# Kernel tuning notes

Hardware: AMD Instinct MI355X
Metric: run time of the kernel (lower is better)

Reference implementation:

```python
import jax, jax.numpy as jnp
import numpy as np

B, N, C, H = 16, 577, 768, 12
KEEP_RATE = 0.7


def setup_inputs() -> dict:
    key = jax.random.key(0)
    k1, k2, k3 = jax.random.split(key, 3)
    x = jax.random.normal(k1, (B, N, C), dtype=jnp.float32)
    W_qkv = jax.random.normal(k2, (C, 3 * C), dtype=jnp.float32) * 0.02
    W_proj = jax.random.normal(k3, (C, C), dtype=jnp.float32) * 0.02
    b_proj = jnp.zeros((C,), dtype=jnp.float32)
    return {"x": x, "W_qkv": W_qkv, "W_proj": W_proj, "b_proj": b_proj}


def reference(x, W_qkv, W_proj, b_proj):
    b, n, c = x.shape
    h = H
    dh = c // h
    scale = dh ** (-0.5)

    # qkv projection -> q,k,v each [B,H,N,dh]
    qkv = (x @ W_qkv).reshape(b, n, 3, h, dh)
    qkv = jnp.transpose(qkv, (2, 0, 3, 1, 4))
    q, k, v = qkv[0], qkv[1], qkv[2]

    # full attention scores [B,H,N,N] (materialized, as in the source)
    attn = jnp.einsum('bhnd,bhmd->bhnm', q, k) * scale

    # --- top_pool from row-0 (CLS) scores, attn_method == 'SUM_ABS_1' ---
    # attn[:, :, 0, :] -> [B,H,N]; sum |.| over heads -> [B,N] (== mean over C=1 channel)
    attn_weight = jnp.sum(jnp.abs(attn[:, :, 0, :]), axis=1)  # [B,N]
    # exclude_first=True: drop CLS, topk over remaining N-1, alpha1=1, alpha2=0 (C==1 -> std=0)
    w = attn_weight[:, 1:]                       # [B, N-1]
    keep_num = max(int((n - 1) * KEEP_RATE), 1)  # static
    _, idx = jax.lax.top_k(w, keep_num)          # [B, keep_num]
    idx = jnp.sort(idx, axis=1)
    idx = jnp.concatenate(
        [jnp.zeros((b, 1), dtype=idx.dtype), idx + 1], axis=1)  # prepend CLS index 0
    # expand to [B, keep_num+1, dim] as in torch (pool dim kwarg == self.dim)
    keep_index = jnp.broadcast_to(idx[:, :, None], (b, keep_num + 1, c))

    # standard attention output
    a = jax.nn.softmax(attn, axis=-1)
    out = jnp.einsum('bhnm,bhmd->bhnd', a, v)    # [B,H,N,dh]
    out = jnp.transpose(out, (0, 2, 1, 3)).reshape(b, n, c)
    out = out @ W_proj + b_proj
    return out, keep_index
```

## Files before the change

### kernel.cpp

```cpp
#include <hip/hip_runtime.h>
#include <hip/hip_bf16.h>
#include <stdint.h>

#define B_    16
#define N_    577
#define C_    768
#define H_    12
#define M_    (B_*N_)
#define QKVN  (3*C_)
#define NKEEP 403
#define KROWS (NKEEP+1)
#define VTLD  640
#define PTLD  72

typedef short s16x8 __attribute__((ext_vector_type(8)));
typedef float f32x4 __attribute__((ext_vector_type(4)));

__device__ __forceinline__ unsigned short f2bf(float x){
  unsigned int u = __float_as_uint(x);
  u += 0x7FFF + ((u >> 16) & 1);
  return (unsigned short)(u >> 16);
}

__device__ __forceinline__ void gld_lds16(const void* g, void* l){
  __builtin_amdgcn_global_load_lds(
      (const __attribute__((address_space(1))) unsigned int*)g,
      (__attribute__((address_space(3))) unsigned int*)l, 16, 0, 0);
}

template<int NT, int M9, int MTILES>
__device__ __forceinline__ void tile_map(int L, int& mt, int& nt){
  constexpr int NB = MTILES*NT;
  int x = L & 7, j = L >> 3;
  if(j < M9*NT){
    nt = j/M9; mt = x*M9 + (j - nt*M9);
  } else {
    int offt = 0;
    #pragma unroll
    for(int y=0;y<8;y++) if(y<x) offt += ((NB-1-y)>>3) + 1 - M9*NT;
    int ft = offt + (j - M9*NT);
    mt = 8*M9 + ft/NT;
    nt = ft - (ft/NT)*NT;
  }
}

__global__ __launch_bounds__(256) void k_prep(const float* __restrict__ x,
                       const float* __restrict__ Wqkv, const float* __restrict__ Wproj,
                       unsigned short* __restrict__ xb, unsigned short* __restrict__ wqkvT,
                       unsigned short* __restrict__ wprojT, float* __restrict__ qcls){
  __shared__ float tile[64][65];
  __shared__ float part[4][64];
  const int bid = blockIdx.x, t = threadIdx.x;
  if(bid < 6924){
    int i = bid*256 + t;
    float4 v = ((const float4*)x)[i];
    ushort4 o; o.x=f2bf(v.x); o.y=f2bf(v.y); o.z=f2bf(v.z); o.w=f2bf(v.w);
    ((ushort4*)xb)[i] = o;
  } else if(bid < 7500){
    const float* in; unsigned short* out; int R, CC, bx, by;
    if(bid < 7356){ int r = bid - 6924; bx = r % 36; by = r / 36; in = Wqkv;  out = wqkvT;  R = 768; CC = 2304; }
    else          { int r = bid - 7356; bx = r % 12; by = r / 12; in = Wproj; out = wprojT; R = 768; CC = 768;  }
    int r0 = by*64, c0 = bx*64;
    int tx = t & 63, ty = t >> 6;
    #pragma unroll
    for(int i=0;i<16;i++){
      int r = ty + i*4;
      tile[r][tx] = in[(size_t)(r0+r)*CC + c0 + tx];
    }
    __syncthreads();
    #pragma unroll
    for(int i=0;i<16;i++){
      int c = ty + i*4;
      out[(size_t)(c0+c)*R + r0 + tx] = f2bf(tile[tx][c]);
    }
  } else {
    int r = bid - 7500;
    const int b = r / 12, j0 = (r % 12)*64;
    float* xs = &tile[0][0];
    const float* xr = x + (size_t)b*577*768;
    xs[t] = xr[t]; xs[t+256] = xr[t+256]; xs[t+512] = xr[t+512];
    __syncthreads();
    const int jl = t & 63, cs = t >> 6;
    float acc = 0.f;
    const float* wp = Wqkv + (size_t)(cs*192)*2304 + j0 + jl;
    #pragma unroll 4
    for(int c=0;c<192;c++){ acc += xs[cs*192+c] * wp[0]; wp += 2304; }
    part[cs][jl] = acc;
    __syncthreads();
    if(t < 64) qcls[b*768 + j0 + t] = part[0][t]+part[1][t]+part[2][t]+part[3][t];
  }
}

template<int LDC_, bool BF16OUT, bool FUSEV, int NT>
__global__ __launch_bounds__(256) void k_gemm_bt(const unsigned short* __restrict__ A,
                          const unsigned short* __restrict__ Bt,
                          void* __restrict__ Cout,
                          const float* __restrict__ bias, int Mdim,
                          unsigned short* __restrict__ vtbuf){
  __shared__ __align__(16) unsigned short As[128*32];
  __shared__ __align__(16) unsigned short Bs[128*32];
  const int t = threadIdx.x;
  const int w = t>>6, l = t&63, lq = l>>4, lr = l&15;
  const int wm = w>>1, wn = w&1;
  int mt, nt; tile_map<NT, 9, 73>(blockIdx.x, mt, nt);
  const int m0 = mt*128, n0 = nt*128;
  int rA0 = m0 + (t>>2);       if(rA0 >= Mdim) rA0 = Mdim-1;
  int rA1 = m0 + ((t+256)>>2); if(rA1 >= Mdim) rA1 = Mdim-1;
  const unsigned short* gA0 = A  + (size_t)rA0*768 + (t&3)*8;
  const unsigned short* gA1 = A  + (size_t)rA1*768 + (t&3)*8;
  const unsigned short* gB0 = Bt + (size_t)(n0 + (t>>2))*768 + (t&3)*8;
  const unsigned short* gB1 = Bt + (size_t)(n0 + ((t+256)>>2))*768 + (t&3)*8;
  unsigned short* lA0 = As + (size_t)w*512;
  unsigned short* lA1 = As + 2048 + (size_t)w*512;
  unsigned short* lB0 = Bs + (size_t)w*512;
  unsigned short* lB1 = Bs + 2048 + (size_t)w*512;
  f32x4 acc[4][4] = {};
  for(int kt=0; kt<24; ++kt){
    const int ko = kt*32;
    __syncthreads();
    gld_lds16(gA0 + ko, lA0); gld_lds16(gA1 + ko, lA1);
    gld_lds16(gB0 + ko, lB0); gld_lds16(gB1 + ko, lB1);
    __syncthreads();
    s16x8 af[4], bfr[4];
    #pragma unroll
    for(int it=0;it<4;it++) af[it]  = *(const s16x8*)&As[(wm*64+it*16+lr)*32 + lq*8];
    #pragma unroll
    for(int jt=0;jt<4;jt++) bfr[jt] = *(const s16x8*)&Bs[(wn*64+jt*16+lr)*32 + lq*8];
    #pragma unroll
    for(int it=0;it<4;it++)
      #pragma unroll
      for(int jt=0;jt<4;jt++)
        acc[it][jt] = __builtin_amdgcn_mfma_f32_16x16x32_bf16(af[it], bfr[jt], acc[it][jt], 0,0,0);
  }
  if(FUSEV && n0 >= 1536){
    #pragma unroll
    for(int it=0;it<4;it++){
      int tok0 = m0 + wm*64 + it*16 + lq*4;
      #pragma unroll
      for(int jt=0;jt<4;jt++){
        int vrow = (n0 - 1536) + wn*64 + jt*16 + lr;
        ushort4 pk; unsigned short* pks = (unsigned short*)&pk;
        #pragma unroll
        for(int r=0;r<4;r++) pks[r] = f2bf(acc[it][jt][r]);
        int b0 = tok0/577, t0 = tok0 - b0*577;
        if(tok0 + 3 < M_ && t0 + 3 < 577){
          *(ushort4*)&vtbuf[(size_t)(b0*768 + vrow)*VTLD + t0] = pk;
        } else {
          #pragma unroll
          for(int r=0;r<4;r++){
            int tg = tok0 + r;
            if(tg < M_){
              int bb = tg/577, tt = tg - bb*577;
              vtbuf[(size_t)(bb*768 + vrow)*VTLD + tt] = pks[r];
            }
          }
        }
      }
    }
  } else {
    #pragma unroll
    for(int it=0;it<4;it++){
      #pragma unroll
      for(int r=0;r<4;r++){
        int row = m0 + wm*64 + it*16 + lq*4 + r;
        if(row < Mdim){
          #pragma unroll
          for(int jt=0;jt<4;jt++){
            int col = n0 + wn*64 + jt*16 + lr;
            float v = acc[it][jt][r];
            if constexpr (BF16OUT)
              ((unsigned short*)Cout)[(size_t)row*LDC_ + col] = f2bf(v);
            else
              ((float*)Cout)[(size_t)row*LDC_ + col] = v + bias[col];
          }
        }
      }
    }
  }
}

template<int LDC_, bool BF16OUT, bool FUSEV, int NT>
__global__ __launch_bounds__(256) void k_gemm_bt_k64(const unsigned short* __restrict__ A,
                          const unsigned short* __restrict__ Bt,
                          void* __restrict__ Cout,
                          const float* __restrict__ bias, int Mdim,
                          unsigned short* __restrict__ vtbuf){
  __shared__ __align__(16) unsigned short As[128*64];
  __shared__ __align__(16) unsigned short Bs[128*64];
  const int t = threadIdx.x;
  const int w = t>>6, l = t&63, lq = l>>4, lr = l&15;
  const int wm = w>>1, wn = w&1;
  int mt, nt; tile_map<NT, 9, 73>(blockIdx.x, mt, nt);
  const int m0 = mt*128, n0 = nt*128;
  const int srow = t>>3;
  const int csw  = (((t&7) ^ ((t>>3)&7))<<3);
  const unsigned short* gA[4]; const unsigned short* gB[4];
  #pragma unroll
  for(int i=0;i<4;i++){
    int ra = m0 + i*32 + srow; if(ra >= Mdim) ra = Mdim-1;
    gA[i] = A  + (size_t)ra*768 + csw;
    gB[i] = Bt + (size_t)(n0 + i*32 + srow)*768 + csw;
  }
  unsigned short* dA = As + (size_t)w*512;
  unsigned short* dB = Bs + (size_t)w*512;
  const int rxa = lr&7;
  f32x4 acc[4][4] = {};
  for(int kt=0; kt<12; ++kt){
    const int ko = kt*64;
    __syncthreads();
    #pragma unroll
    for(int i=0;i<4;i++){
      gld_lds16(gA[i] + ko, dA + i*2048);
      gld_lds16(gB[i] + ko, dB + i*2048);
    }
    __syncthreads();
    #pragma unroll
    for(int ks=0;ks<2;ks++){
      s16x8 af[4], bfr[4];
      const int cx = ((ks*4 + lq) ^ rxa) << 3;
      #pragma unroll
      for(int it=0;it<4;it++) af[it]  = *(const s16x8*)&As[(wm*64+it*16+lr)*64 + cx];
      #pragma unroll
      for(int jt=0;jt<4;jt++) bfr[jt] = *(const s16x8*)&Bs[(wn*64+jt*16+lr)*64 + cx];
      #pragma unroll
      for(int it=0;it<4;it++)
        #pragma unroll
        for(int jt=0;jt<4;jt++)
          acc[it][jt] = __builtin_amdgcn_mfma_f32_16x16x32_bf16(af[it], bfr[jt], acc[it][jt], 0,0,0);
    }
  }
  if(FUSEV && n0 >= 1536){
    #pragma unroll
    for(int it=0;it<4;it++){
      int tok0 = m0 + wm*64 + it*16 + lq*4;
      #pragma unroll
      for(int jt=0;jt<4;jt++){
        int vrow = (n0 - 1536) + wn*64 + jt*16 + lr;
        ushort4 pk; unsigned short* pks = (unsigned short*)&pk;
        #pragma unroll
        for(int r=0;r<4;r++) pks[r] = f2bf(acc[it][jt][r]);
        int b0 = tok0/577, t0 = tok0 - b0*577;
        if(tok0 + 3 < M_ && t0 + 3 < 577){
          *(ushort4*)&vtbuf[(size_t)(b0*768 + vrow)*VTLD + t0] = pk;
        } else {
          #pragma unroll
          for(int r=0;r<4;r++){
            int tg = tok0 + r;
            if(tg < M_){
              int bb = tg/577, tt = tg - bb*577;
              vtbuf[(size_t)(bb*768 + vrow)*VTLD + tt] = pks[r];
            }
          }
        }
      }
    }
  } else {
    #pragma unroll
    for(int it=0;it<4;it++){
      #pragma unroll
      for(int r=0;r<4;r++){
        int row = m0 + wm*64 + it*16 + lq*4 + r;
        if(row < Mdim){
          #pragma unroll
          for(int jt=0;jt<4;jt++){
            int col = n0 + wn*64 + jt*16 + lr;
            float v = acc[it][jt][r];
            if constexpr (BF16OUT)
              ((unsigned short*)Cout)[(size_t)row*LDC_ + col] = f2bf(v);
            else
              ((float*)Cout)[(size_t)row*LDC_ + col] = v + bias[col];
          }
        }
      }
    }
  }
}

__global__ __launch_bounds__(256,4) void k_attn(const unsigned short* __restrict__ qkv,
                                                const unsigned short* __restrict__ vtbuf,
                                                unsigned short* __restrict__ aout){
  __shared__ __align__(16) unsigned short Ks[64*64];
  __shared__ __align__(16) unsigned short Vt[64*64];
  __shared__ __align__(16) unsigned short Ptt[128*PTLD];
  __shared__ float Ls[4][2][16][4];
  const int blk = blockIdx.x;
  const int bh = blk % 192, qt = blk / 192;
  const int b = bh / 12, h = bh % 12;
  const int t = threadIdx.x, w = t>>6, l = t&63, lq = l>>4, lr = l&15;
  const size_t base = (size_t)(b*577)*2304 + h*64;
  const int q0 = qt*128;
  s16x8 bq[2][2];
  #pragma unroll
  for(int it=0;it<2;it++){
    int qrow = q0 + w*32 + it*16 + lr; if(qrow > 576) qrow = 576;
    #pragma unroll
    for(int ks=0;ks<2;ks++)
      bq[it][ks] = *(const s16x8*)&qkv[base + (size_t)qrow*2304 + ks*32 + lq*8];
  }
  const int srow = w*8 + (l>>3);
  const int cswz8 = (((l&7) ^ (l>>3)) << 3);
  unsigned short* ldsK = Ks + w*512 + l*8;
  unsigned short* ldsV = Vt + w*512 + l*8;
  const unsigned short* gVbase = vtbuf + (size_t)(bh*64)*VTLD + cswz8;

  f32x4 acc_o[2][4] = {};
  float lsum[2] = {0.f, 0.f};
  const float CEXP = 0.18033688011112043f;

  s16x8 kreg0, kreg1, vreg0, vreg1;
  auto stage_issue = [&](int tt){
    const int j0i = tt*64;
    int kr0 = j0i + srow;      if(kr0 > 576) kr0 = 576;
    int kr1 = j0i + 32 + srow; if(kr1 > 576) kr1 = 576;
    kreg0 = *(const s16x8*)(qkv + base + 768 + (size_t)kr0*2304 + cswz8);
    kreg1 = *(const s16x8*)(qkv + base + 768 + (size_t)kr1*2304 + cswz8);
    vreg0 = *(const s16x8*)(gVbase + (size_t)srow*VTLD + j0i);
    vreg1 = *(const s16x8*)(gVbase + (size_t)(32 + srow)*VTLD + j0i);
  };

  stage_issue(0);
  for(int g=0; g<10; ++g){
    const int j0 = g*64;
    const bool edge = (g == 9);
    *(s16x8*)(ldsK)        = kreg0;
    *(s16x8*)(ldsK + 2048) = kreg1;
    *(s16x8*)(ldsV)        = vreg0;
    *(s16x8*)(ldsV + 2048) = vreg1;
    asm volatile("s_waitcnt lgkmcnt(0)" ::: "memory");
    __builtin_amdgcn_s_barrier();
    __builtin_amdgcn_sched_barrier(0);
    if(g < 9) stage_issue(g+1);

    f32x4 accs[2][4] = {};
    #pragma unroll
    for(int ks=0;ks<2;ks++){
      s16x8 ak[4];
      #pragma unroll
      for(int jt=0;jt<4;jt++){
        int j = jt*16 + lr;
        ak[jt] = *(const s16x8*)&Ks[j*64 + (((4*ks+lq) ^ (j&7))<<3)];
      }
      #pragma unroll
      for(int it=0;it<2;it++)
        #pragma unroll
        for(int jt=0;jt<4;jt++)
          accs[it][jt] = __builtin_amdgcn_mfma_f32_16x16x32_bf16(ak[jt], bq[it][ks], accs[it][jt], 0,0,0);
    }
    #pragma unroll
    for(int it=0;it<2;it++){
      int qlocal = w*32 + it*16 + lr;
      #pragma unroll
      for(int jt=0;jt<4;jt++){
        ushort4 pk;
        unsigned short* pks = (unsigned short*)&pk;
        #pragma unroll
        for(int r=0;r<4;r++){
          float p = exp2f(accs[it][jt][r] * CEXP);
          if(edge){ if(j0 + jt*16 + lq*4 + r > 576) p = 0.f; }
          lsum[it] += p;
          pks[r] = f2bf(p);
        }
        *(ushort4*)&Ptt[qlocal*PTLD + jt*16 + lq*4] = pk;
      }
    }
    #pragma unroll
    for(int ks=0;ks<2;ks++){
      s16x8 ap[2], bv[4];
      #pragma unroll
      for(int it=0;it<2;it++)
        ap[it] = *(const s16x8*)&Ptt[(w*32+it*16+lr)*PTLD + ks*32 + lq*8];
      #pragma unroll
      for(int dt=0;dt<4;dt++){
        int d = dt*16 + lr;
        bv[dt] = *(const s16x8*)&Vt[d*64 + (((4*ks+lq) ^ (d&7))<<3)];
      }
      #pragma unroll
      for(int it=0;it<2;it++)
        #pragma unroll
        for(int dt=0;dt<4;dt++)
          acc_o[it][dt] = __builtin_amdgcn_mfma_f32_16x16x32_bf16(ap[it], bv[dt], acc_o[it][dt], 0,0,0);
    }
    asm volatile("s_waitcnt lgkmcnt(0)" ::: "memory");
    __builtin_amdgcn_s_barrier();
    __builtin_amdgcn_sched_barrier(0);
  }

  #pragma unroll
  for(int it=0;it<2;it++) Ls[w][it][lr][lq] = lsum[it];
  #pragma unroll
  for(int it=0;it<2;it++){
    #pragma unroll
    for(int r=0;r<4;r++){
      int n = q0 + w*32 + it*16 + lq*4 + r;
      if(n <= 576){
        int q16 = lq*4 + r;
        float lt = Ls[w][it][q16][0] + Ls[w][it][q16][1] + Ls[w][it][q16][2] + Ls[w][it][q16][3];
        float inv = 1.f / lt;
        #pragma unroll
        for(int dt=0;dt<4;dt++)
          aout[(size_t)(b*577+n)*768 + h*64 + dt*16 + lr] = f2bf(acc_o[it][dt][r]*inv);
      }
    }
  }
}

__global__ void k_u(const float* __restrict__ Wqkv, const float* __restrict__ qcls,
                    float* __restrict__ u){
  int h = blockIdx.x, b = blockIdx.y, c = threadIdx.x;
  const float* qc = qcls + b*768 + h*64;
  const float* wr = Wqkv + (size_t)c*2304 + 768 + h*64;
  float acc = 0.f;
  #pragma unroll
  for(int d=0;d<64;d++) acc += wr[d]*qc[d];
  u[(size_t)(b*12+h)*768 + c] = acc;
}
__global__ void k_attw(const float* __restrict__ x, const float* __restrict__ u,
                       float* __restrict__ attw){
  int blk = blockIdx.x;
  int b = blk/577, m = blk%577;
  int lane = threadIdx.x;
  const float* xr = x + (size_t)(b*577+m)*768;
  const float* ub = u + (size_t)b*12*768;
  float part[12];
  #pragma unroll
  for(int h=0;h<12;h++) part[h]=0.f;
  #pragma unroll
  for(int i=0;i<12;i++){
    float xv = xr[i*64 + lane];
    #pragma unroll
    for(int h=0;h<12;h++) part[h] += xv * ub[h*768 + i*64 + lane];
  }
  float s = 0.f;
  #pragma unroll
  for(int h=0;h<12;h++){
    float v = part[h];
    #pragma unroll
    for(int off=32; off; off>>=1) v += __shfl_xor(v, off);
    s += fabsf(v);
  }
  if(lane==0) attw[b*577 + m] = 0.125f * s;
}
__global__ void k_topk_fill(const float* __restrict__ attw, float* __restrict__ out2){
  __shared__ float sw[576];
  __shared__ int wtot[9];
  __shared__ int sidx[KROWS];
  int b = blockIdx.x, t = threadIdx.x;
  float wv = attw[b*577 + 1 + t];
  sw[t] = wv;
  __syncthreads();
  int rank = 0;
  for(int j=0;j<576;j++){
    float wj = sw[j];
    rank += (wj > wv) || (wj == wv && j < t);
  }
  bool kept = rank < NKEEP;
  unsigned long long mask = __ballot(kept);
  int wid = t>>6, lane = t&63;
  int pos = __popcll(mask & ((1ull<<lane)-1ull));
  if(lane==0) wtot[wid] = __popcll(mask);
  __syncthreads();
  int off0 = 0;
  for(int q=0;q<wid;q++) off0 += wtot[q];
  if(kept) sidx[1 + off0 + pos] = t+1;
  if(t==0) sidx[0] = 0;
  __syncthreads();
  float4* o4 = (float4*)out2 + (size_t)b*KROWS*192;
  for(int i = t; i < KROWS*192; i += 576){
    float v = (float)sidx[i/192];
    o4[i] = make_float4(v,v,v,v);
  }
}

extern "C" void kernel_launch(void* const* d_in, const int* in_sizes, int n_in,
                              void* d_out, int out_size, void* d_ws, size_t ws_size,
                              hipStream_t stream){
  const float* x     = (const float*)d_in[0];
  const float* Wqkv  = (const float*)d_in[1];
  const float* Wproj = (const float*)d_in[2];
  const float* bias  = (const float*)d_in[3];
  float* out  = (float*)d_out;
  float* out2 = out + (size_t)M_*768;

  char* ws = (char*)d_ws;
  size_t off = 0;
  auto alloc = [&](size_t bytes)->void*{ void* p = ws + off; off += (bytes + 255) & ~(size_t)255; return p; };
  unsigned short* xb     = (unsigned short*)alloc((size_t)M_*768*2);
  unsigned short* wqkvT  = (unsigned short*)alloc((size_t)QKVN*768*2);
  unsigned short* wprojT = (unsigned short*)alloc((size_t)768*768*2);
  unsigned short* qkvb   = (unsigned short*)alloc((size_t)M_*QKVN*2);
  unsigned short* aoutb  = (unsigned short*)alloc((size_t)M_*768*2);
  unsigned short* vtbuf  = (unsigned short*)alloc((size_t)192*64*VTLD*2);
  float* qcls   = (float*)alloc((size_t)16*768*4);
  float* u      = (float*)alloc((size_t)16*12*768*4);
  float* attw   = (float*)alloc((size_t)16*577*4);

  k_prep<<<7692, 256, 0, stream>>>(x, Wqkv, Wproj, xb, wqkvT, wprojT, qcls);
  k_gemm_bt_k64<QKVN, true, true, 18><<<73*18, 256, 0, stream>>>(xb, wqkvT, qkvb, nullptr, M_, vtbuf);
  k_u<<<dim3(12,16), 768, 0, stream>>>(Wqkv, qcls, u);
  k_attw<<<16*577, 64, 0, stream>>>(x, u, attw);
  k_topk_fill<<<16, 576, 0, stream>>>(attw, out2);
  k_attn<<<960, 256, 0, stream>>>(qkvb, vtbuf, aoutb);
  k_gemm_bt<768, false, false, 6><<<73*6, 256, 0, stream>>>(aoutb, wprojT, out, bias, M_, nullptr);
}
```

Baseline: 271.5 us.

## Double-buffer QKV GEMM with async LDS prefetch and switch proj GEMM to k64

Adds a double-buffered GEMM kernel that prefetches the next two 64-wide K slices straight into LDS while MFMAs run on the current slice. It uses explicit vmcnt waits, raw barriers and setprio to keep the compute and load phases overlapped. The QKV projection moves to this kernel. The output projection moves from the older 32-wide-K kernel to the existing k64 swizzled kernel, and the shared epilogue is factored into a helper. The cost is twice the LDS per block (64KB), which may reduce occupancy.

```diff
diff --git a/kernel.cpp b/kernel.cpp
--- a/kernel.cpp
+++ b/kernel.cpp
@@ -91,47 +91,10 @@
   }
 }
 
-template<int LDC_, bool BF16OUT, bool FUSEV, int NT>
-__global__ __launch_bounds__(256) void k_gemm_bt(const unsigned short* __restrict__ A,
-                          const unsigned short* __restrict__ Bt,
-                          void* __restrict__ Cout,
-                          const float* __restrict__ bias, int Mdim,
-                          unsigned short* __restrict__ vtbuf){
-  __shared__ __align__(16) unsigned short As[128*32];
-  __shared__ __align__(16) unsigned short Bs[128*32];
-  const int t = threadIdx.x;
-  const int w = t>>6, l = t&63, lq = l>>4, lr = l&15;
-  const int wm = w>>1, wn = w&1;
-  int mt, nt; tile_map<NT, 9, 73>(blockIdx.x, mt, nt);
-  const int m0 = mt*128, n0 = nt*128;
-  int rA0 = m0 + (t>>2);       if(rA0 >= Mdim) rA0 = Mdim-1;
-  int rA1 = m0 + ((t+256)>>2); if(rA1 >= Mdim) rA1 = Mdim-1;
-  const unsigned short* gA0 = A  + (size_t)rA0*768 + (t&3)*8;
-  const unsigned short* gA1 = A  + (size_t)rA1*768 + (t&3)*8;
-  const unsigned short* gB0 = Bt + (size_t)(n0 + (t>>2))*768 + (t&3)*8;
-  const unsigned short* gB1 = Bt + (size_t)(n0 + ((t+256)>>2))*768 + (t&3)*8;
-  unsigned short* lA0 = As + (size_t)w*512;
-  unsigned short* lA1 = As + 2048 + (size_t)w*512;
-  unsigned short* lB0 = Bs + (size_t)w*512;
-  unsigned short* lB1 = Bs + 2048 + (size_t)w*512;
-  f32x4 acc[4][4] = {};
-  for(int kt=0; kt<24; ++kt){
-    const int ko = kt*32;
-    __syncthreads();
-    gld_lds16(gA0 + ko, lA0); gld_lds16(gA1 + ko, lA1);
-    gld_lds16(gB0 + ko, lB0); gld_lds16(gB1 + ko, lB1);
-    __syncthreads();
-    s16x8 af[4], bfr[4];
-    #pragma unroll
-    for(int it=0;it<4;it++) af[it]  = *(const s16x8*)&As[(wm*64+it*16+lr)*32 + lq*8];
-    #pragma unroll
-    for(int jt=0;jt<4;jt++) bfr[jt] = *(const s16x8*)&Bs[(wn*64+jt*16+lr)*32 + lq*8];
-    #pragma unroll
-    for(int it=0;it<4;it++)
-      #pragma unroll
-      for(int jt=0;jt<4;jt++)
-        acc[it][jt] = __builtin_amdgcn_mfma_f32_16x16x32_bf16(af[it], bfr[jt], acc[it][jt], 0,0,0);
-  }
+template<int LDC_, bool BF16OUT, bool FUSEV>
+__device__ __forceinline__ void gemm_epilogue(f32x4 (&acc)[4][4], int m0, int n0,
+                          int wm, int wn, int lq, int lr, void* Cout,
+                          const float* bias, int Mdim, unsigned short* vtbuf){
   if(FUSEV && n0 >= 1536){
     #pragma unroll
     for(int it=0;it<4;it++){
@@ -229,51 +192,82 @@
           acc[it][jt] = __builtin_amdgcn_mfma_f32_16x16x32_bf16(af[it], bfr[jt], acc[it][jt], 0,0,0);
     }
   }
-  if(FUSEV && n0 >= 1536){
-    #pragma unroll
-    for(int it=0;it<4;it++){
-      int tok0 = m0 + wm*64 + it*16 + lq*4;
-      #pragma unroll
-      for(int jt=0;jt<4;jt++){
-        int vrow = (n0 - 1536) + wn*64 + jt*16 + lr;
-        ushort4 pk; unsigned short* pks = (unsigned short*)&pk;
-        #pragma unroll
-        for(int r=0;r<4;r++) pks[r] = f2bf(acc[it][jt][r]);
-        int b0 = tok0/577, t0 = tok0 - b0*577;
-        if(tok0 + 3 < M_ && t0 + 3 < 577){
-          *(ushort4*)&vtbuf[(size_t)(b0*768 + vrow)*VTLD + t0] = pk;
-        } else {
-          #pragma unroll
-          for(int r=0;r<4;r++){
-            int tg = tok0 + r;
-            if(tg < M_){
-              int bb = tg/577, tt = tg - bb*577;
-              vtbuf[(size_t)(bb*768 + vrow)*VTLD + tt] = pks[r];
-            }
-          }
-        }
-      }
-    }
-  } else {
-    #pragma unroll
-    for(int it=0;it<4;it++){
-      #pragma unroll
-      for(int r=0;r<4;r++){
-        int row = m0 + wm*64 + it*16 + lq*4 + r;
-        if(row < Mdim){
-          #pragma unroll
-          for(int jt=0;jt<4;jt++){
-            int col = n0 + wn*64 + jt*16 + lr;
-            float v = acc[it][jt][r];
-            if constexpr (BF16OUT)
-              ((unsigned short*)Cout)[(size_t)row*LDC_ + col] = f2bf(v);
-            else
-              ((float*)Cout)[(size_t)row*LDC_ + col] = v + bias[col];
-          }
-        }
-      }
-    }
-  }
+  gemm_epilogue<LDC_, BF16OUT, FUSEV>(acc, m0, n0, wm, wn, lq, lr, Cout, bias, Mdim, vtbuf);
+}
+
+template<int LDC_, bool BF16OUT, bool FUSEV, int NT>
+__global__ __launch_bounds__(256) void k_gemm_db(const unsigned short* __restrict__ A,
+                          const unsigned short* __restrict__ Bt,
+                          void* __restrict__ Cout,
+                          const float* __restrict__ bias, int Mdim,
+                          unsigned short* __restrict__ vtbuf){
+  __shared__ __align__(16) unsigned short As[2][128*64];
+  __shared__ __align__(16) unsigned short Bs[2][128*64];
+  const int t = threadIdx.x;
+  const int w = t>>6, l = t&63, lq = l>>4, lr = l&15;
+  const int wm = w>>1, wn = w&1;
+  int mt, nt; tile_map<NT, 9, 73>(blockIdx.x, mt, nt);
+  const int m0 = mt*128, n0 = nt*128;
+  const int srow = t>>3;
+  const int csw  = (((t&7) ^ ((t>>3)&7))<<3);
+  const unsigned short* gA[4]; const unsigned short* gB[4];
+  #pragma unroll
+  for(int i=0;i<4;i++){
+    int ra = m0 + i*32 + srow; if(ra >= Mdim) ra = Mdim-1;
+    gA[i] = A  + (size_t)ra*768 + csw;
+    gB[i] = Bt + (size_t)(n0 + i*32 + srow)*768 + csw;
+  }
+  const int rxa = lr&7;
+  f32x4 acc[4][4] = {};
+
+#define STAGE_DB(KT, S) do{ \
+  unsigned short* dA_ = &As[(S)][w*512]; \
+  unsigned short* dB_ = &Bs[(S)][w*512]; \
+  _Pragma("unroll") \
+  for(int i_=0;i_<4;i_++){ \
+    gld_lds16(gA[i_] + (size_t)(KT)*64, dA_ + i_*2048); \
+    gld_lds16(gB[i_] + (size_t)(KT)*64, dB_ + i_*2048); \
+  } \
+}while(0)
+
+  STAGE_DB(0,0);
+  STAGE_DB(1,1);
+  asm volatile("s_waitcnt vmcnt(8)" ::: "memory");
+  __builtin_amdgcn_s_barrier();
+
+  for(int kt=0; kt<12; ++kt){
+    const int s = kt&1;
+    s16x8 af[4][2], bfr[4][2];
+    #pragma unroll
+    for(int ks=0;ks<2;ks++){
+      const int cx = ((ks*4 + lq) ^ rxa) << 3;
+      #pragma unroll
+      for(int it=0;it<4;it++) af[it][ks]  = *(const s16x8*)&As[s][(wm*64+it*16+lr)*64 + cx];
+      #pragma unroll
+      for(int jt=0;jt<4;jt++) bfr[jt][ks] = *(const s16x8*)&Bs[s][(wn*64+jt*16+lr)*64 + cx];
+    }
+    asm volatile("s_waitcnt lgkmcnt(0)" ::: "memory");
+    __builtin_amdgcn_sched_barrier(0);
+    __builtin_amdgcn_s_barrier();
+    if(kt<10) STAGE_DB(kt+2, s);
+    __builtin_amdgcn_s_setprio(1);
+    #pragma unroll
+    for(int ks=0;ks<2;ks++)
+      #pragma unroll
+      for(int it=0;it<4;it++)
+        #pragma unroll
+        for(int jt=0;jt<4;jt++)
+          acc[it][jt] = __builtin_amdgcn_mfma_f32_16x16x32_bf16(af[it][ks], bfr[jt][ks], acc[it][jt], 0,0,0);
+    __builtin_amdgcn_s_setprio(0);
+    if(kt<10){
+      asm volatile("s_waitcnt vmcnt(8)" ::: "memory");
+    } else if(kt==10){
+      asm volatile("s_waitcnt vmcnt(0)" ::: "memory");
+    }
+    __builtin_amdgcn_s_barrier();
+  }
+  gemm_epilogue<LDC_, BF16OUT, FUSEV>(acc, m0, n0, wm, wn, lq, lr, Cout, bias, Mdim, vtbuf);
+#undef STAGE_DB
 }
 
 __global__ __launch_bounds__(256,4) void k_attn(const unsigned short* __restrict__ qkv,
@@ -495,10 +489,10 @@
   float* attw   = (float*)alloc((size_t)16*577*4);
 
   k_prep<<<7692, 256, 0, stream>>>(x, Wqkv, Wproj, xb, wqkvT, wprojT, qcls);
-  k_gemm_bt_k64<QKVN, true, true, 18><<<73*18, 256, 0, stream>>>(xb, wqkvT, qkvb, nullptr, M_, vtbuf);
+  k_gemm_db<QKVN, true, true, 18><<<73*18, 256, 0, stream>>>(xb, wqkvT, qkvb, nullptr, M_, vtbuf);
   k_u<<<dim3(12,16), 768, 0, stream>>>(Wqkv, qcls, u);
   k_attw<<<16*577, 64, 0, stream>>>(x, u, attw);
   k_topk_fill<<<16, 576, 0, stream>>>(attw, out2);
   k_attn<<<960, 256, 0, stream>>>(qkvb, vtbuf, aoutb);
-  k_gemm_bt<768, false, false, 6><<<73*6, 256, 0, stream>>>(aoutb, wprojT, out, bias, M_, nullptr);
-}
+  k_gemm_bt_k64<768, false, false, 6><<<73*6, 256, 0, stream>>>(aoutb, wprojT, out, bias, M_, nullptr);
+}
```

New measurement: 268.7 us, median of 2. No clear change (-1.1%).
